# Kernel tuning notes

Hardware: AMD Instinct MI355X
Metric: run time of the kernel (lower is better)

The kernel has to match this reference:

```python
import jax, jax.numpy as jnp
import numpy as np

B, S, E, H = 4, 2048, 512, 8
D = E // H  # head dim = 64
# Faithful to torch precedence bug: embed_dim // num_heads ** 0.5 == E // (H**0.5)
SCALE = float(E // H ** 0.5)  # 181.0
EPS = 1e-5


def _ln(x, g, b):
    mu = jnp.mean(x, axis=-1, keepdims=True)
    var = jnp.var(x, axis=-1, keepdims=True)
    return (x - mu) / jnp.sqrt(var + EPS) * g + b


def setup_inputs() -> dict:
    key = jax.random.key(0)
    ks = jax.random.split(key, 14)
    inv = 1.0 / np.sqrt(E)
    inp = {
        'q': jax.random.normal(ks[0], (B, S, E), jnp.float32),
        'k': jax.random.normal(ks[1], (B, S, E), jnp.float32),
        'v': jax.random.normal(ks[2], (B, S, E), jnp.float32),
        'Wq': jax.random.uniform(ks[3], (E, E), jnp.float32, -inv, inv),
        'bq': jnp.zeros((E,), jnp.float32),
        'Wk': jax.random.uniform(ks[4], (E, E), jnp.float32, -inv, inv),
        'bk': jnp.zeros((E,), jnp.float32),
        'Wv': jax.random.uniform(ks[5], (E, E), jnp.float32, -inv, inv),
        'bv': jnp.zeros((E,), jnp.float32),
        'Wo': jax.random.uniform(ks[6], (E, E), jnp.float32, -inv, inv),
        'bo': jnp.zeros((E,), jnp.float32),
        'gq': jnp.ones((D,), jnp.float32), 'betaq': jnp.zeros((D,), jnp.float32),
        'gk': jnp.ones((D,), jnp.float32), 'betak': jnp.zeros((D,), jnp.float32),
        'gv': jnp.ones((D,), jnp.float32), 'betav': jnp.zeros((D,), jnp.float32),
        'query_mask': jax.random.uniform(ks[7], (B, S, 1)) < 0.9,
        'key_mask': jax.random.uniform(ks[8], (B, S, 1)) < 0.9,
        'value_mask': jax.random.uniform(ks[9], (B, S, 1)) < 0.9,
    }
    return inp


def reference(q, k, v, Wq, bq, Wk, bk, Wv, bv, Wo, bo,
              gq, betaq, gk, betak, gv, betav,
              query_mask, key_mask, value_mask):
    # project + mask (bool mask multiplies as 0/1)
    qp = (q @ Wq.T + bq) * query_mask            # [B,S,E]
    kp = (k @ Wk.T + bk) * key_mask
    vp = (v @ Wv.T + bv) * value_mask
    # split heads -> [B,H,S,D]
    split = lambda x: x.reshape(B, -1, H, D).transpose(0, 2, 1, 3)
    qh, kh, vh = split(qp), split(kp), split(vp)
    # middle_norm: per-head LayerNorm over head dim
    qh, kh, vh = _ln(qh, gq, betaq), _ln(kh, gk, betak), _ln(vh, gv, betav)
    scores = jnp.einsum('bhqd,bhkd->bhqk', qh, kh) / SCALE  # [B,H,S,S]
    km = key_mask[:, :, 0][:, None, None, :]     # [B,1,1,S]
    scores = jnp.where(km, scores, -1e9)
    attn = jax.nn.softmax(scores, axis=-1)
    qm = query_mask[:, :, 0][:, None, :, None]   # [B,1,S,1]
    attn = attn * qm                              # zero-fill post-softmax
    out = jnp.einsum('bhqk,bhkd->bhqd', attn, vh)
    out = out.transpose(0, 2, 1, 3).reshape(B, -1, E)
    out = (out @ Wo.T + bo) * query_mask
    return out
```

## Files before the change

### kernel.cpp

```cpp
#include <hip/hip_runtime.h>
#include <cstdint>
#include <cstddef>

#define BB 4
#define SS 2048
#define EE 512
#define HH 8
#define DD 64
#define MM (BB*SS)
#define BHSD ((size_t)BB*HH*SS*DD)

static constexpr float SCALE_INV = 1.0f / 181.0f;
static constexpr float LOG2E = 1.4426950408889634f;
static constexpr float LN_EPS = 1e-5f;

typedef float  v4f  __attribute__((ext_vector_type(4)));
typedef __bf16 v8bf __attribute__((ext_vector_type(8)));
typedef __bf16 v4bf __attribute__((ext_vector_type(4)));
typedef short  s4   __attribute__((ext_vector_type(4)));

static __device__ __forceinline__ v4f mfma16(v8bf a, v8bf b, v4f c) {
  return __builtin_amdgcn_mfma_f32_16x16x32_bf16(a, b, c, 0, 0, 0);
}

static __device__ __forceinline__ float fexp2(float x) {
#if __has_builtin(__builtin_amdgcn_exp2f)
  return __builtin_amdgcn_exp2f(x);
#else
  return __expf(x * 0.6931471805599453f);
#endif
}

typedef const void __attribute__((address_space(1))) gas_void;
typedef void __attribute__((address_space(3))) las_void;
static __device__ __forceinline__ void gload_lds16(const void* g, void* l) {
  __builtin_amdgcn_global_load_lds((gas_void*)g, (las_void*)l, 16, 0, 0);
}

static constexpr size_t oXb = 0;
static constexpr size_t oWb = oXb + (size_t)3*MM*EE*2;
static constexpr size_t oXh = oWb + (size_t)4*EE*EE*2;
static constexpr size_t oAO = oXh + (size_t)3*MM*EE*2;
static constexpr size_t oMk = oAO + (size_t)MM*EE*2;

__global__ void mask_kernel(const void* qm, const void* km, const void* vm, float* maskF) {
  __shared__ int s_n01, s_nF;
  const int t = threadIdx.x;
  if (t == 0) { s_n01 = 0; s_nF = 0; }
  __syncthreads();
  int n01 = 0, nF = 0;
  const unsigned* wq = (const unsigned*)qm;
  for (int i = t; i < 2048; i += 256) {
    const unsigned u = wq[i];
    if (u != 0u && u != 1u) n01 = 1;
    if (u != 0u && u != 0x3F800000u) nF = 1;
  }
  if (n01) atomicOr(&s_n01, 1);
  if (nF)  atomicOr(&s_nF, 1);
  __syncthreads();
  const int mode = (!s_n01) ? 0 : (!s_nF) ? 1 : 2;
  const int gidx = blockIdx.x * 256 + t;
  const int m = gidx / MM, i = gidx % MM;
  const void* p = (m == 0) ? qm : (m == 1) ? km : vm;
  int v;
  if (mode == 0)      v = (((const int*)p)[i] != 0);
  else if (mode == 1) v = (((const unsigned*)p)[i] != 0u);
  else                v = (((const unsigned char*)p)[i] != 0);
  maskF[m*MM + i] = v ? 1.0f : 0.0f;
}

__global__ void convert_kernel(const float* q, const float* k, const float* v,
                               const float* Wq, const float* Wk, const float* Wv, const float* Wo,
                               __bf16* Xb, __bf16* Wb) {
  const long idx = (long)blockIdx.x * 256 + threadIdx.x;
  const long NX4 = (long)3*MM*EE/4;
  const long NW4 = (long)4*EE*EE/4;
  if (idx < NX4) {
    const long per = (long)MM*EE/4;
    const long mat = idx / per, off = idx % per;
    const float* src = (mat == 0) ? q : (mat == 1) ? k : v;
    v4f val = ((const v4f*)src)[off];
    v4bf o; o[0]=(__bf16)val[0]; o[1]=(__bf16)val[1]; o[2]=(__bf16)val[2]; o[3]=(__bf16)val[3];
    ((v4bf*)Xb)[idx] = o;
  } else if (idx < NX4 + NW4) {
    const long j = idx - NX4;
    const long per = (long)EE*EE/4;
    const long mat = j / per, off = j % per;
    const float* src = (mat == 0) ? Wq : (mat == 1) ? Wk : (mat == 2) ? Wv : Wo;
    v4f val = ((const v4f*)src)[off];
    v4bf o; o[0]=(__bf16)val[0]; o[1]=(__bf16)val[1]; o[2]=(__bf16)val[2]; o[3]=(__bf16)val[3];
    ((v4bf*)Wb)[j] = o;
  }
}

__global__ __launch_bounds__(256) void gemm_proj_ln(const __bf16* Xb, const __bf16* Wb,
                                                    const float* bq, const float* bk, const float* bv,
                                                    const float* gq, const float* betaq,
                                                    const float* gk, const float* betak,
                                                    const float* gv, const float* betav,
                                                    const float* maskF, __bf16* Xh) {
  const int m0  = blockIdx.x * 128;
  const int n0  = blockIdx.y * 128;
  const int mat = blockIdx.z;
  const __bf16* A = Xb + (size_t)mat*MM*EE;
  const __bf16* W = Wb + (size_t)mat*EE*EE;
  const float* bias = (mat == 0) ? bq : (mat == 1) ? bk : bv;
  const float* gam  = (mat == 0) ? gq : (mat == 1) ? gk : gv;
  const float* bet  = (mat == 0) ? betaq : (mat == 1) ? betak : betav;

  __shared__ char smem[32768];

  const int t = threadIdx.x;
  const int lane = t & 63, w = t >> 6;
  const int wm = w >> 1, wn = w & 1;
  const int l15 = lane & 15, lg = lane >> 4;

  v4f acc[4][4];
  const v4f zf = {0.f, 0.f, 0.f, 0.f};
#pragma unroll
  for (int i = 0; i < 4; ++i)
#pragma unroll
    for (int j = 0; j < 4; ++j) acc[i][j] = zf;

  const int sr0 = (w*64 + lane) >> 2;
  const int sct = (w*64 + lane) & 3;
#define STAGE_PL(BUF, KT)                                                                 \
  {                                                                                       \
    char* ab_ = (BUF);                                                                    \
    char* bb_ = (BUF) + 8192;                                                             \
    _Pragma("unroll")                                                                     \
    for (int j_ = 0; j_ < 2; ++j_) {                                                      \
      const int r_ = sr0 + j_*64;                                                         \
      const int c_ = sct ^ (r_ & 3);                                                      \
      gload_lds16(A + (size_t)(m0 + r_)*EE + (KT) + c_*8, ab_ + j_*4096 + w*1024);        \
      gload_lds16(W + (size_t)(n0 + r_)*EE + (KT) + c_*8, bb_ + j_*4096 + w*1024);        \
    }                                                                                     \
  }

  char* buf0 = smem;
  char* buf1 = smem + 16384;

  STAGE_PL(buf0, 0);
  __syncthreads();

  int cur = 0;
  for (int kt = 0; kt < EE; kt += 32) {
    char* cb = cur ? buf1 : buf0;
    char* nb = cur ? buf0 : buf1;
    if (kt + 32 < EE) STAGE_PL(nb, kt + 32);

    const char* As = cb;
    const char* Bs = cb + 8192;
    v8bf afr[4], bfr[4];
#pragma unroll
    for (int i = 0; i < 4; ++i) {
      const int ra = wm*64 + i*16 + l15;
      afr[i] = *(const v8bf*)(As + ra*64 + ((16*lg) ^ ((ra & 3) << 4)));
      const int rb = wn*64 + i*16 + l15;
      bfr[i] = *(const v8bf*)(Bs + rb*64 + ((16*lg) ^ ((rb & 3) << 4)));
    }
#pragma unroll
    for (int i = 0; i < 4; ++i)
#pragma unroll
      for (int j = 0; j < 4; ++j)
        acc[i][j] = mfma16(afr[i], bfr[j], acc[i][j]);
    __syncthreads();
    cur ^= 1;
  }
#undef STAGE_PL

  const int nbase = n0 + wn*64;
  const int h = nbase >> 6;
  float bsv[4], gmv[4], btv[4];
#pragma unroll
  for (int j = 0; j < 4; ++j) {
    const int d = j*16 + l15;
    bsv[j] = bias[nbase + d];
    gmv[j] = gam[d];
    btv[j] = bet[d];
  }
#pragma unroll
  for (int i = 0; i < 4; ++i)
#pragma unroll
    for (int rr = 0; rr < 4; ++rr) {
      const int row = m0 + wm*64 + i*16 + 4*lg + rr;
      const float mv = maskF[mat*MM + row];
      float x[4];
      float s = 0.f, s2 = 0.f;
#pragma unroll
      for (int j = 0; j < 4; ++j) {
        x[j] = (acc[i][j][rr] + bsv[j]) * mv;
        s += x[j]; s2 += x[j]*x[j];
      }
      s  += __shfl_xor(s, 1, 64);  s  += __shfl_xor(s, 2, 64);
      s  += __shfl_xor(s, 4, 64);  s  += __shfl_xor(s, 8, 64);
      s2 += __shfl_xor(s2, 1, 64); s2 += __shfl_xor(s2, 2, 64);
      s2 += __shfl_xor(s2, 4, 64); s2 += __shfl_xor(s2, 8, 64);
      const float mu  = s * (1.0f/64.0f);
      const float var = s2 * (1.0f/64.0f) - mu*mu;
      const float rstd = rsqrtf(var + LN_EPS);
      const int bidx = row >> 11, sI = row & 2047;
      if (mat == 2) {
        const size_t vbase = 2*BHSD + (((size_t)bidx*HH + h)*DD)*SS;
#pragma unroll
        for (int j = 0; j < 4; ++j)
          Xh[vbase + (size_t)(j*16 + l15)*SS + sI] = (__bf16)((x[j] - mu)*rstd*gmv[j] + btv[j]);
      } else {
        const size_t base = (size_t)mat*BHSD + (((size_t)bidx*HH + h)*SS + sI)*DD;
#pragma unroll
        for (int j = 0; j < 4; ++j)
          Xh[base + j*16 + l15] = (__bf16)((x[j] - mu)*rstd*gmv[j] + btv[j]);
      }
    }
}

__global__ __launch_bounds__(512) void attn_kernel(const __bf16* Xh, const float* maskF, __bf16* AO) {
  const int bid = blockIdx.x;
  const int xcd = bid & 7;
  const int slot = bid >> 3;
  const int qb = slot & 15;
  const int g = xcd + 8*(slot >> 4);
  const int b = g >> 3, h = g & 7;

  const int t = threadIdx.x;
  const int w = t >> 6, lane = t & 63;
  const int hh = w >> 2, wq = w & 3;
  const int l15 = lane & 15, lg = lane >> 4;

  __shared__ char smem[65536];

  const size_t headoff = (((size_t)b*HH + h)*SS)*DD;
  const __bf16* Qg = Xh + headoff;
  const __bf16* Kg = Xh + BHSD + headoff;
  const __bf16* Vt = Xh + 2*BHSD + (((size_t)b*HH + h)*DD)*SS;
  const float* qmF = maskF + (size_t)b*SS;
  const float* kmF = maskF + MM + (size_t)b*SS;

  const int q0 = qb*128 + wq*32;

  v8bf qf[2][2];
#pragma unroll
  for (int m = 0; m < 2; ++m)
#pragma unroll
    for (int kd = 0; kd < 2; ++kd) {
      v8bf r = *(const v8bf*)(Qg + (size_t)(q0 + m*16 + l15)*DD + kd*32 + lg*8);
      v8bf o;
#pragma unroll
      for (int e = 0; e < 8; ++e) o[e] = (__bf16)((float)r[e] * (SCALE_INV * LOG2E));
      qf[m][kd] = o;
    }

  v8bf onesb;
#pragma unroll
  for (int e = 0; e < 8; ++e) onesb[e] = (__bf16)1.0f;

  v4f O[2][4];
  v4f lacc[2];
  const v4f zf = {0.f,0.f,0.f,0.f};
#pragma unroll
  for (int m = 0; m < 2; ++m) {
    lacc[m] = zf;
#pragma unroll
    for (int df = 0; df < 4; ++df) O[m][df] = zf;
  }

  const int srow = lane >> 3;
  const int sc   = lane & 7;
#define SIGMA(r) (((r) & ~31) | ((((r)>>2)&3)<<3) | ((((r)>>4)&1)<<2) | ((r)&3))
#define STAGE1(BUFC, KT0)                                                                  \
  {                                                                                        \
    char* kb_ = (BUFC);                                                                    \
    char* vb_ = (BUFC) + 8192;                                                             \
    _Pragma("unroll")                                                                      \
    for (int j_ = 0; j_ < 2; ++j_) {                                                       \
      const int r0_ = wq*16 + j_*8;                                                        \
      const int r_  = r0_ + srow;                                                          \
      const int sg_ = SIGMA(r_);                                                           \
      gload_lds16(Kg + (size_t)((KT0) + sg_)*DD + ((sc ^ (r_ & 7))*8), kb_ + r0_*128);     \
      gload_lds16(Vt + (size_t)r_*SS + (KT0) + ((sc ^ (r_ & 7))*8),  vb_ + r0_*128);       \
    }                                                                                      \
  }

  char* bufA = smem + hh*32768;
  char* bufB = bufA + 16384;

  STAGE1(bufA, hh*64);
  __syncthreads();

  for (int tt = 0; tt < 16; ++tt) {
    char* cur = (tt & 1) ? bufB : bufA;
    char* nxt = (tt & 1) ? bufA : bufB;
    if (tt + 1 < 16) STAGE1(nxt, ((tt+1)*2 + hh)*64);

    const int kt0 = (tt*2 + hh)*64;
    char* kb = cur;
    char* vb = cur + 8192;

    v8bf kf[4][2];
#pragma unroll
    for (int f = 0; f < 4; ++f)
#pragma unroll
      for (int kd = 0; kd < 2; ++kd) {
        const int rr = f*16 + l15;
        kf[f][kd] = *(const v8bf*)(kb + rr*128 + (((kd*4 + lg) ^ (rr & 7))*16));
      }

    v4f st[2][4];
#pragma unroll
    for (int m = 0; m < 2; ++m)
#pragma unroll
      for (int f = 0; f < 4; ++f) st[m][f] = zf;
#pragma unroll
    for (int kd = 0; kd < 2; ++kd)
#pragma unroll
      for (int f = 0; f < 4; ++f)
#pragma unroll
        for (int m = 0; m < 2; ++m)
          st[m][f] = mfma16(kf[f][kd], qf[m][kd], st[m][f]);

    v4f km4[4];
#pragma unroll
    for (int f = 0; f < 4; ++f)
      km4[f] = *(const v4f*)(kmF + kt0 + (f >> 1)*32 + (f & 1)*4 + 8*lg);

#pragma unroll
    for (int m = 0; m < 2; ++m) {
      float p[4][4];
#pragma unroll
      for (int f = 0; f < 4; ++f)
#pragma unroll
        for (int rr = 0; rr < 4; ++rr)
          p[f][rr] = fexp2(st[m][f][rr]) * km4[f][rr];
#pragma unroll
      for (int g2 = 0; g2 < 2; ++g2) {
        v8bf pa;
        pa[0] = (__bf16)p[2*g2][0];   pa[1] = (__bf16)p[2*g2][1];
        pa[2] = (__bf16)p[2*g2][2];   pa[3] = (__bf16)p[2*g2][3];
        pa[4] = (__bf16)p[2*g2+1][0]; pa[5] = (__bf16)p[2*g2+1][1];
        pa[6] = (__bf16)p[2*g2+1][2]; pa[7] = (__bf16)p[2*g2+1][3];
        lacc[m] = mfma16(pa, onesb, lacc[m]);
#pragma unroll
        for (int df = 0; df < 4; ++df) {
          const int rv = df*16 + l15;
          v8bf vv = *(const v8bf*)(vb + rv*128 + (((g2*4 + lg) ^ (rv & 7))*16));
          O[m][df] = mfma16(pa, vv, O[m][df]);
        }
      }
    }
    __syncthreads();
  }
#undef STAGE1
#undef SIGMA

  float (*Pp)[32][65] = (float (*)[32][65])smem;
  float (*Lp)[32]     = (float (*)[32])(smem + 4*32*65*4);
  if (hh == 1) {
#pragma unroll
    for (int m = 0; m < 2; ++m)
#pragma unroll
      for (int df = 0; df < 4; ++df)
#pragma unroll
        for (int rr = 0; rr < 4; ++rr)
          Pp[wq][m*16 + 4*lg + rr][df*16 + l15] = O[m][df][rr];
    if (l15 == 0) {
#pragma unroll
      for (int m = 0; m < 2; ++m)
#pragma unroll
        for (int rr = 0; rr < 4; ++rr)
          Lp[wq][m*16 + 4*lg + rr] = lacc[m][rr];
    }
  }
  __syncthreads();
  if (hh == 0) {
#pragma unroll
    for (int m = 0; m < 2; ++m)
#pragma unroll
      for (int df = 0; df < 4; ++df)
#pragma unroll
        for (int rr = 0; rr < 4; ++rr)
          O[m][df][rr] += Pp[wq][m*16 + 4*lg + rr][df*16 + l15];
#pragma unroll
    for (int m = 0; m < 2; ++m)
#pragma unroll
      for (int rr = 0; rr < 4; ++rr) {
        const float lr = lacc[m][rr] + Lp[wq][m*16 + 4*lg + rr];
        const int qrow = q0 + m*16 + 4*lg + rr;
        const float scl = qmF[qrow] / fmaxf(lr, 1e-30f);
#pragma unroll
        for (int df = 0; df < 4; ++df)
          AO[(size_t)(b*SS + qrow)*EE + h*DD + df*16 + l15] = (__bf16)(O[m][df][rr] * scl);
      }
  }
}

__global__ __launch_bounds__(256) void gemm_out(const __bf16* AO, const __bf16* Wb,
                                                const float* bo, const float* maskF, float* out) {
  const int m0 = blockIdx.x * 128;
  const int n0 = blockIdx.y * 128;
  const __bf16* A = AO;
  const __bf16* W = Wb + (size_t)3*EE*EE;

  __shared__ char smem[32768];

  const int t = threadIdx.x;
  const int lane = t & 63, w = t >> 6;
  const int wm = w >> 1, wn = w & 1;
  const int l15 = lane & 15, lg = lane >> 4;

  v4f acc[4][4];
  const v4f zf = {0.f,0.f,0.f,0.f};
#pragma unroll
  for (int i = 0; i < 4; ++i)
#pragma unroll
    for (int j = 0; j < 4; ++j) acc[i][j] = zf;

  const int sr0 = (w*64 + lane) >> 2;
  const int sct = (w*64 + lane) & 3;
#define STAGE_PL(BUF, KT)                                                                 \
  {                                                                                       \
    char* ab_ = (BUF);                                                                    \
    char* bb_ = (BUF) + 8192;                                                             \
    _Pragma("unroll")                                                                     \
    for (int j_ = 0; j_ < 2; ++j_) {                                                      \
      const int r_ = sr0 + j_*64;                                                         \
      const int c_ = sct ^ (r_ & 3);                                                      \
      gload_lds16(A + (size_t)(m0 + r_)*EE + (KT) + c_*8, ab_ + j_*4096 + w*1024);        \
      gload_lds16(W + (size_t)(n0 + r_)*EE + (KT) + c_*8, bb_ + j_*4096 + w*1024);        \
    }                                                                                     \
  }

  char* buf0 = smem;
  char* buf1 = smem + 16384;

  STAGE_PL(buf0, 0);
  __syncthreads();

  int cur = 0;
  for (int kt = 0; kt < EE; kt += 32) {
    char* cb = cur ? buf1 : buf0;
    char* nb = cur ? buf0 : buf1;
    if (kt + 32 < EE) STAGE_PL(nb, kt + 32);

    const char* As = cb;
    const char* Bs = cb + 8192;
    v8bf afr[4], bfr[4];
#pragma unroll
    for (int i = 0; i < 4; ++i) {
      const int ra = wm*64 + i*16 + l15;
      afr[i] = *(const v8bf*)(As + ra*64 + ((16*lg) ^ ((ra & 3) << 4)));
      const int rb = wn*64 + i*16 + l15;
      bfr[i] = *(const v8bf*)(Bs + rb*64 + ((16*lg) ^ ((rb & 3) << 4)));
    }
#pragma unroll
    for (int i = 0; i < 4; ++i)
#pragma unroll
      for (int j = 0; j < 4; ++j)
        acc[i][j] = mfma16(afr[i], bfr[j], acc[i][j]);
    __syncthreads();
    cur ^= 1;
  }
#undef STAGE_PL

  float bsv[4]; int ncol[4];
#pragma unroll
  for (int j = 0; j < 4; ++j) {
    ncol[j] = n0 + wn*64 + j*16 + l15;
    bsv[j] = bo[ncol[j]];
  }
#pragma unroll
  for (int i = 0; i < 4; ++i)
#pragma unroll
    for (int rr = 0; rr < 4; ++rr) {
      const int row = m0 + wm*64 + i*16 + 4*lg + rr;
      const float mv = maskF[row];
#pragma unroll
      for (int j = 0; j < 4; ++j)
        out[(size_t)row*EE + ncol[j]] = (acc[i][j][rr] + bsv[j]) * mv;
    }
}

extern "C" void kernel_launch(void* const* d_in, const int* in_sizes, int n_in,
                              void* d_out, int out_size, void* d_ws, size_t ws_size,
                              hipStream_t stream) {
  const float* q  = (const float*)d_in[0];
  const float* k  = (const float*)d_in[1];
  const float* v  = (const float*)d_in[2];
  const float* Wq = (const float*)d_in[3];
  const float* bq = (const float*)d_in[4];
  const float* Wk = (const float*)d_in[5];
  const float* bk = (const float*)d_in[6];
  const float* Wv = (const float*)d_in[7];
  const float* bv = (const float*)d_in[8];
  const float* Wo = (const float*)d_in[9];
  const float* bo = (const float*)d_in[10];
  const float* gq = (const float*)d_in[11];
  const float* betaq = (const float*)d_in[12];
  const float* gk = (const float*)d_in[13];
  const float* betak = (const float*)d_in[14];
  const float* gv = (const float*)d_in[15];
  const float* betav = (const float*)d_in[16];

  char* ws = (char*)d_ws;
  __bf16* Xb = (__bf16*)(ws + oXb);
  __bf16* Wb = (__bf16*)(ws + oWb);
  __bf16* Xh = (__bf16*)(ws + oXh);
  __bf16* AO = (__bf16*)(ws + oAO);
  float*  maskF = (float*)(ws + oMk);

  mask_kernel<<<dim3(96), dim3(256), 0, stream>>>(d_in[17], d_in[18], d_in[19], maskF);
  convert_kernel<<<dim3(13312), dim3(256), 0, stream>>>(q, k, v, Wq, Wk, Wv, Wo, Xb, Wb);
  gemm_proj_ln<<<dim3(64, 4, 3), dim3(256), 0, stream>>>(Xb, Wb, bq, bk, bv,
                                                         gq, betaq, gk, betak, gv, betav,
                                                         maskF, Xh);
  attn_kernel<<<dim3(512), dim3(512), 0, stream>>>(Xh, maskF, AO);
  gemm_out<<<dim3(64, 4, 1), dim3(256), 0, stream>>>(AO, Wb, bo, maskF, (float*)d_out);
}
```

Baseline: 114.9 us.

## Fuse fp32-to-bf16 activation conversion into projection GEMM staging

Drops the separate pass that converted q/k/v activations to bf16. The projection GEMM now streams fp32 activations straight into shared memory through async global-to-LDS loads, using a new XOR swizzle, and converts them to bf16 while building the MFMA fragments. This removes a full read and write of the bf16 activation copies and shrinks the convert kernel to weights only. In exchange the GEMM reads twice as many activation bytes per tile, needs more LDS (48KB, which may lower occupancy), and adds conversion instructions to its inner loop.

```diff
diff --git a/kernel.cpp b/kernel.cpp
--- a/kernel.cpp
+++ b/kernel.cpp
@@ -37,8 +37,7 @@
   __builtin_amdgcn_global_load_lds((gas_void*)g, (las_void*)l, 16, 0, 0);
 }
 
-static constexpr size_t oXb = 0;
-static constexpr size_t oWb = oXb + (size_t)3*MM*EE*2;
+static constexpr size_t oWb = 0;
 static constexpr size_t oXh = oWb + (size_t)4*EE*EE*2;
 static constexpr size_t oAO = oXh + (size_t)3*MM*EE*2;
 static constexpr size_t oMk = oAO + (size_t)MM*EE*2;
@@ -69,31 +68,19 @@
   maskF[m*MM + i] = v ? 1.0f : 0.0f;
 }
 
-__global__ void convert_kernel(const float* q, const float* k, const float* v,
-                               const float* Wq, const float* Wk, const float* Wv, const float* Wo,
-                               __bf16* Xb, __bf16* Wb) {
-  const long idx = (long)blockIdx.x * 256 + threadIdx.x;
-  const long NX4 = (long)3*MM*EE/4;
-  const long NW4 = (long)4*EE*EE/4;
-  if (idx < NX4) {
-    const long per = (long)MM*EE/4;
-    const long mat = idx / per, off = idx % per;
-    const float* src = (mat == 0) ? q : (mat == 1) ? k : v;
-    v4f val = ((const v4f*)src)[off];
-    v4bf o; o[0]=(__bf16)val[0]; o[1]=(__bf16)val[1]; o[2]=(__bf16)val[2]; o[3]=(__bf16)val[3];
-    ((v4bf*)Xb)[idx] = o;
-  } else if (idx < NX4 + NW4) {
-    const long j = idx - NX4;
-    const long per = (long)EE*EE/4;
-    const long mat = j / per, off = j % per;
-    const float* src = (mat == 0) ? Wq : (mat == 1) ? Wk : (mat == 2) ? Wv : Wo;
-    v4f val = ((const v4f*)src)[off];
-    v4bf o; o[0]=(__bf16)val[0]; o[1]=(__bf16)val[1]; o[2]=(__bf16)val[2]; o[3]=(__bf16)val[3];
-    ((v4bf*)Wb)[j] = o;
-  }
-}
-
-__global__ __launch_bounds__(256) void gemm_proj_ln(const __bf16* Xb, const __bf16* Wb,
+__global__ void convert_kernel(const float* Wq, const float* Wk, const float* Wv, const float* Wo,
+                               __bf16* Wb) {
+  const long j = (long)blockIdx.x * 256 + threadIdx.x;
+  const long per = (long)EE*EE/4;
+  const long mat = j / per, off = j % per;
+  const float* src = (mat == 0) ? Wq : (mat == 1) ? Wk : (mat == 2) ? Wv : Wo;
+  v4f val = ((const v4f*)src)[off];
+  v4bf o; o[0]=(__bf16)val[0]; o[1]=(__bf16)val[1]; o[2]=(__bf16)val[2]; o[3]=(__bf16)val[3];
+  ((v4bf*)Wb)[j] = o;
+}
+
+__global__ __launch_bounds__(256) void gemm_proj_ln(const float* Aq, const float* Ak, const float* Av,
+                                                    const __bf16* Wb,
                                                     const float* bq, const float* bk, const float* bv,
                                                     const float* gq, const float* betaq,
                                                     const float* gk, const float* betak,
@@ -102,13 +89,13 @@
   const int m0  = blockIdx.x * 128;
   const int n0  = blockIdx.y * 128;
   const int mat = blockIdx.z;
-  const __bf16* A = Xb + (size_t)mat*MM*EE;
+  const float* A = (mat == 0) ? Aq : (mat == 1) ? Ak : Av;
   const __bf16* W = Wb + (size_t)mat*EE*EE;
   const float* bias = (mat == 0) ? bq : (mat == 1) ? bk : bv;
   const float* gam  = (mat == 0) ? gq : (mat == 1) ? gk : gv;
   const float* bet  = (mat == 0) ? betaq : (mat == 1) ? betak : betav;
 
-  __shared__ char smem[32768];
+  __shared__ char smem[49152];
 
   const int t = threadIdx.x;
   const int lane = t & 63, w = t >> 6;
@@ -127,18 +114,25 @@
 #define STAGE_PL(BUF, KT)                                                                 \
   {                                                                                       \
     char* ab_ = (BUF);                                                                    \
-    char* bb_ = (BUF) + 8192;                                                             \
+    char* bb_ = (BUF) + 16384;                                                            \
     _Pragma("unroll")                                                                     \
-    for (int j_ = 0; j_ < 2; ++j_) {                                                      \
+    for (int j_ = 0; j_ < 4; ++j_) {                      \
+      const int fl_ = j_*256 + w*64 + lane;                                               \
+      const int r_  = fl_ >> 3;                                                           \
+      const int s_  = fl_ & 7;                                                            \
+      const int c_  = s_ ^ (r_ & 7);                                                      \
+      gload_lds16(A + (size_t)(m0 + r_)*EE + (KT) + c_*4, ab_ + (j_*4 + w)*1024);         \
+    }                                                                                     \
+    _Pragma("unroll")                                                                     \
+    for (int j_ = 0; j_ < 2; ++j_) {                      \
       const int r_ = sr0 + j_*64;                                                         \
       const int c_ = sct ^ (r_ & 3);                                                      \
-      gload_lds16(A + (size_t)(m0 + r_)*EE + (KT) + c_*8, ab_ + j_*4096 + w*1024);        \
       gload_lds16(W + (size_t)(n0 + r_)*EE + (KT) + c_*8, bb_ + j_*4096 + w*1024);        \
     }                                                                                     \
   }
 
   char* buf0 = smem;
-  char* buf1 = smem + 16384;
+  char* buf1 = smem + 24576;
 
   STAGE_PL(buf0, 0);
   __syncthreads();
@@ -150,12 +144,19 @@
     if (kt + 32 < EE) STAGE_PL(nb, kt + 32);
 
     const char* As = cb;
-    const char* Bs = cb + 8192;
+    const char* Bs = cb + 16384;
     v8bf afr[4], bfr[4];
 #pragma unroll
     for (int i = 0; i < 4; ++i) {
       const int ra = wm*64 + i*16 + l15;
-      afr[i] = *(const v8bf*)(As + ra*64 + ((16*lg) ^ ((ra & 3) << 4)));
+      const int c0 = (2*lg) ^ (ra & 7);
+      const int c1 = (2*lg + 1) ^ (ra & 7);
+      v4f f0 = *(const v4f*)(As + ra*128 + c0*16);
+      v4f f1 = *(const v4f*)(As + ra*128 + c1*16);
+      v8bf a;
+      a[0]=(__bf16)f0[0]; a[1]=(__bf16)f0[1]; a[2]=(__bf16)f0[2]; a[3]=(__bf16)f0[3];
+      a[4]=(__bf16)f1[0]; a[5]=(__bf16)f1[1]; a[6]=(__bf16)f1[2]; a[7]=(__bf16)f1[3];
+      afr[i] = a;
       const int rb = wn*64 + i*16 + l15;
       bfr[i] = *(const v8bf*)(Bs + rb*64 + ((16*lg) ^ ((rb & 3) << 4)));
     }
@@ -501,15 +502,14 @@
   const float* betav = (const float*)d_in[16];
 
   char* ws = (char*)d_ws;
-  __bf16* Xb = (__bf16*)(ws + oXb);
   __bf16* Wb = (__bf16*)(ws + oWb);
   __bf16* Xh = (__bf16*)(ws + oXh);
   __bf16* AO = (__bf16*)(ws + oAO);
   float*  maskF = (float*)(ws + oMk);
 
   mask_kernel<<<dim3(96), dim3(256), 0, stream>>>(d_in[17], d_in[18], d_in[19], maskF);
-  convert_kernel<<<dim3(13312), dim3(256), 0, stream>>>(q, k, v, Wq, Wk, Wv, Wo, Xb, Wb);
-  gemm_proj_ln<<<dim3(64, 4, 3), dim3(256), 0, stream>>>(Xb, Wb, bq, bk, bv,
+  convert_kernel<<<dim3(1024), dim3(256), 0, stream>>>(Wq, Wk, Wv, Wo, Wb);
+  gemm_proj_ln<<<dim3(64, 4, 3), dim3(256), 0, stream>>>(q, k, v, Wb, bq, bk, bv,
                                                          gq, betaq, gk, betak, gv, betav,
                                                          maskF, Xh);
   attn_kernel<<<dim3(512), dim3(512), 0, stream>>>(Xh, maskF, AO);
```

Result: faster. 108.6 us (-5.5%).
